# Kernel tuning notes

Hardware: AMD Instinct MI355X
Metric: run time of the kernel (lower is better)

Reference implementation:

```python
import math
import jax, jax.numpy as jnp
import numpy as np

B, T, D_MODEL = 4, 2048, 1024
H, HD = 16, 64            # head_dim = d_model // n_heads
NF = 128                  # n_features
EPS = 1e-6
INV_SQRT_NF = 1.0 / math.sqrt(NF)


def make_orf(key, head_dim, n_features, dtype=jnp.float32):
    """Orthogonal Random Features: QR-orthogonalized gaussian blocks, scaled by sqrt(d)."""
    n_blocks = math.ceil(n_features / head_dim)
    keys = jax.random.split(key, n_blocks)
    blocks = []
    for k in keys:
        g = jax.random.normal(k, (head_dim, head_dim), dtype)
        qm, _ = jnp.linalg.qr(g)
        blocks.append(qm)
    W = jnp.concatenate(blocks, axis=1)[:, :n_features]
    return W * jnp.asarray(math.sqrt(head_dim), dtype)


def setup_inputs() -> dict:
    key = jax.random.key(0)
    k0, k1, k2, k3, k4, k5 = jax.random.split(key, 6)
    s = 1.0 / math.sqrt(D_MODEL)  # torch Linear default init scale
    x = jax.random.normal(k0, (B, T, D_MODEL), jnp.float32)
    Wq = jax.random.uniform(k1, (D_MODEL, H * HD), jnp.float32, -s, s)
    Wk = jax.random.uniform(k2, (D_MODEL, H * HD), jnp.float32, -s, s)
    Wv = jax.random.uniform(k3, (D_MODEL, H * HD), jnp.float32, -s, s)
    Wo = jax.random.uniform(k4, (H * HD, D_MODEL), jnp.float32, -s, s)
    W_feat = make_orf(k5, HD, NF)  # (HD, NF), fresh random buffer (not learned)
    return {"x": x, "Wq": Wq, "Wk": Wk, "Wv": Wv, "Wo": Wo, "W_feat": W_feat}


def _favor_plus(x, W):
    """phi(x) = exp(x.W - ||x||^2/2) / sqrt(NF); x:(B,H,T,HD) -> (B,H,T,NF)."""
    sq = 0.5 * jnp.sum(x * x, axis=-1, keepdims=True)
    return jnp.exp(x @ W - sq) * INV_SQRT_NF


def _causal_linear_attention(qp, kp, v):
    """Causal linear attention scan. qp,kp:(B,H,T,NF), v:(B,H,T,HD) -> (B,H,T,HD)."""
    Bb, Hh = qp.shape[0], qp.shape[1]

    def step(carry, qkv):
        S, z = carry  # S:(B,H,NF,HD), z:(B,H,NF)
        q_t, k_t, v_t = qkv
        S = S + jnp.einsum('bhd,bhe->bhde', k_t, v_t)
        z = z + k_t
        num = jnp.einsum('bhd,bhde->bhe', q_t, S)
        den = jnp.einsum('bhd,bhd->bh', q_t, z) + EPS
        return (S, z), num / den[..., None]

    S0 = jnp.zeros((Bb, Hh, NF, HD), qp.dtype)
    z0 = jnp.zeros((Bb, Hh, NF), qp.dtype)
    xs = (jnp.moveaxis(qp, 2, 0), jnp.moveaxis(kp, 2, 0), jnp.moveaxis(v, 2, 0))
    _, ys = jax.lax.scan(step, (S0, z0), xs)  # ys: (T,B,H,HD)
    return jnp.moveaxis(ys, 0, 2)  # (B,H,T,HD)


def reference(x, Wq, Wk, Wv, Wo, W_feat):
    Bb, Tt, _ = x.shape

    def heads(W):
        return (x @ W).reshape(Bb, Tt, H, HD).transpose(0, 2, 1, 3)  # (B,H,T,HD)

    q, k, v = heads(Wq), heads(Wk), heads(Wv)
    qp = _favor_plus(q, W_feat)
    kp = _favor_plus(k, W_feat)
    y = _causal_linear_attention(qp, kp, v)           # (B,H,T,HD)
    y = y.transpose(0, 2, 1, 3).reshape(Bb, Tt, H * HD)
    return y @ Wo
```

## Files before the change

kernel.cpp:

```cpp
#include <hip/hip_runtime.h>
#include <hip/hip_bf16.h>

typedef unsigned int u32;
typedef unsigned short u16;
typedef __bf16 bf16x8 __attribute__((ext_vector_type(8)));
typedef float f32x4 __attribute__((ext_vector_type(4)));

__device__ __forceinline__ float b2f(u16 s){ union{u32 x; float f;} c; c.x = ((u32)s) << 16; return c.f; }
__device__ __forceinline__ float b2f_lo(u32 u){ union{u32 x; float f;} c; c.x = u << 16; return c.f; }
__device__ __forceinline__ float b2f_hi(u32 u){ union{u32 x; float f;} c; c.x = u & 0xFFFF0000u; return c.f; }
__device__ __forceinline__ u16 f2b(float f){
    union{float f; u32 u;} c; c.f = f;
    u32 r = c.u + 0x7FFFu + ((c.u >> 16) & 1u);
    return (u16)(r >> 16);
}
__device__ __forceinline__ u32 pk(float lo, float hi){
    return (u32)f2b(lo) | ((u32)f2b(hi) << 16);
}
__device__ __forceinline__ void gl_lds16(const u16* g, u16* l){
    __builtin_amdgcn_global_load_lds(
        (const __attribute__((address_space(1))) void*)g,
        (__attribute__((address_space(3))) void*)l, 16, 0, 0);
}
#define BARRIER() do { __builtin_amdgcn_s_barrier(); asm volatile("" ::: "memory"); } while(0)
#define SCB __builtin_amdgcn_sched_barrier(0)
#define LD8(p) (*reinterpret_cast<const bf16x8*>(p))


__global__ __launch_bounds__(256) void tobf16(const float* __restrict__ in, u16* __restrict__ out)
{
    size_t i = ((size_t)blockIdx.x * 256 + threadIdx.x) * 8;
    float4 a = *reinterpret_cast<const float4*>(in + i);
    float4 b = *reinterpret_cast<const float4*>(in + i + 4);
    uint4 v; v.x = pk(a.x, a.y); v.y = pk(a.z, a.w); v.z = pk(b.x, b.y); v.w = pk(b.z, b.w);
    *reinterpret_cast<uint4*>(out + i) = v;
}

__global__ __launch_bounds__(256) void transpose_all(const float* __restrict__ Wq, const float* __restrict__ Wk,
                                                     const float* __restrict__ Wv, const float* __restrict__ Wo,
                                                     u16* __restrict__ WTqkv, u16* __restrict__ WTo)
{
    const float* in; u16* out;
    switch (blockIdx.z){
        case 0:  in = Wq; out = WTqkv;           break;
        case 1:  in = Wk; out = WTqkv + 1048576; break;
        case 2:  in = Wv; out = WTqkv + 2097152; break;
        default: in = Wo; out = WTo;             break;
    }
    __shared__ u16 tile[64][72];
    int kb = blockIdx.x * 64, nb = blockIdx.y * 64, tid = threadIdx.x;
#pragma unroll
    for (int i = 0; i < 2; i++){
        int idx = tid + 256*i; int r = idx >> 3; int c8 = (idx & 7) * 8;
        const float* p = &in[(size_t)(kb + r)*1024 + nb + c8];
        float4 lo = *reinterpret_cast<const float4*>(p);
        float4 hi = *reinterpret_cast<const float4*>(p + 4);
        uint4 v;
        v.x = pk(lo.x, lo.y); v.y = pk(lo.z, lo.w);
        v.z = pk(hi.x, hi.y); v.w = pk(hi.z, hi.w);
        *reinterpret_cast<uint4*>(&tile[r][c8]) = v;
    }
    __syncthreads();
#pragma unroll
    for (int i = 0; i < 2; i++){
        int idx = tid + 256*i; int c = idx >> 3; int r8 = (idx & 7) * 8;
        u32 w[4];
#pragma unroll
        for (int j = 0; j < 4; j++)
            w[j] = (u32)tile[r8 + 2*j][c] | ((u32)tile[r8 + 2*j + 1][c] << 16);
        uint4 v; v.x = w[0]; v.y = w[1]; v.z = w[2]; v.w = w[3];
        *reinterpret_cast<uint4*>(&out[(size_t)(nb + c)*1024 + kb + r8]) = v;
    }
}

template<int MODE>
__global__ __launch_bounds__(512, 2) void gemm_1b(const u16* __restrict__ A, const u16* __restrict__ BT,
                                                  float* __restrict__ outf, u16* __restrict__ outh)
{
    __shared__ u16 lds[2][24576];
    const int tid = threadIdx.x;
    const int l = tid & 63, w = tid >> 6;
    const int wr = w >> 2, wc = w & 3;
    const int fr = l & 15, q = l >> 4;
    const int m0 = blockIdx.x * 128, n0 = blockIdx.y * 256;

    const int srow = tid >> 3;
    const int scol = ((tid & 7) ^ (srow & 7)) << 3;
    const u16* Ag = A  + (size_t)(m0 + srow) * 1024 + scol;
    const u16* Bg = BT + (size_t)(n0 + srow) * 1024 + scol;
    const int sd = tid * 8;

    const int colk0 = (q*8)      ^ ((fr & 7) << 3);
    const int colk1 = (32 + q*8) ^ ((fr & 7) << 3);
    const int aoff = (wr*64 + fr) * 64;
    const int boff = 8192 + (wc*64 + fr) * 64;

    f32x4 acc[4][4] = {};

    auto stgA = [&](int buf, int kt){
#pragma unroll
        for (int i = 0; i < 2; ++i)
            gl_lds16(Ag + (size_t)(i*64)*1024 + kt*64, &lds[buf][i*4096 + sd]);
    };
    auto stgB = [&](int buf, int kt){
#pragma unroll
        for (int j = 0; j < 4; ++j)
            gl_lds16(Bg + (size_t)(j*64)*1024 + kt*64, &lds[buf][8192 + j*4096 + sd]);
    };

    stgA(0, 0); stgB(0, 0); stgA(1, 1);
    asm volatile("s_waitcnt vmcnt(2)" ::: "memory");
    SCB;
    BARRIER();

#pragma unroll 1
    for (int uu = 0; uu < 8; ++uu){
#pragma unroll
        for (int par = 0; par < 2; ++par){
            const int u = 2*uu + par;
            u16* Lb = &lds[par][0];
            bf16x8 af[4][2], bf[4][2];

#pragma unroll
            for (int mt = 0; mt < 4; ++mt){
                af[mt][0] = LD8(Lb + aoff + mt*1024 + colk0);
                af[mt][1] = LD8(Lb + aoff + mt*1024 + colk1);
            }
#pragma unroll
            for (int nt = 0; nt < 4; ++nt){
                bf[nt][0] = LD8(Lb + boff + nt*1024 + colk0);
                bf[nt][1] = LD8(Lb + boff + nt*1024 + colk1);
            }
            if (u < 15) stgB(par ^ 1, u + 1);
            if (u < 14) stgA(par, u + 2);

            __builtin_amdgcn_s_setprio(1);
#pragma unroll
            for (int mt = 0; mt < 4; ++mt)
#pragma unroll
                for (int nt = 0; nt < 4; ++nt){
                    acc[mt][nt] = __builtin_amdgcn_mfma_f32_16x16x32_bf16(af[mt][0], bf[nt][0], acc[mt][nt], 0, 0, 0);
                    acc[mt][nt] = __builtin_amdgcn_mfma_f32_16x16x32_bf16(af[mt][1], bf[nt][1], acc[mt][nt], 0, 0, 0);
                }
            __builtin_amdgcn_s_setprio(0);
            SCB;
            if (u < 14){
                asm volatile("s_waitcnt vmcnt(2)" ::: "memory");
                SCB;
                BARRIER();
            } else if (u == 14){
                asm volatile("s_waitcnt vmcnt(0)" ::: "memory");
                SCB;
                BARRIER();
            }
        }
    }

#pragma unroll
    for (int mt = 0; mt < 4; ++mt){
        int row0 = m0 + wr*64 + mt*16 + q*4;
#pragma unroll
        for (int nt = 0; nt < 4; ++nt){
            int col = n0 + wc*64 + nt*16 + fr;
#pragma unroll
            for (int r = 0; r < 4; ++r){
                float val = acc[mt][nt][r];
                int row = row0 + r;
                if (MODE == 2){
                    outf[(size_t)row*1024 + col] = val;
                } else {
                    int which = col >> 10, colw = col & 1023;
                    int h = colw >> 6, d = colw & 63;
                    int bb = row >> 11, tt = row & 2047;
                    outh[(size_t)which*8388608 + (((size_t)(bb*16 + h))*2048 + tt)*64 + d] = f2b(val);
                }
            }
        }
    }
}

__global__ __launch_bounds__(256) void featmap_mfma(const u16* __restrict__ xh, const float* __restrict__ Wf,
                                                    u16* __restrict__ xp)
{
    __shared__ u16 Xl[128][72];
    __shared__ u16 Wft[128][72];
    __shared__ float sqp[128][8];
    __shared__ float sql[128];
    int tid = threadIdx.x;
    int lane = tid & 63, w = tid >> 6;
    int m = lane & 15, q = lane >> 4;
    const u16* xb = xh + (size_t)blockIdx.x * 128 * 64;
#pragma unroll
    for (int it = 0; it < 4; it++){
        int idx = tid + 256*it;
        int row = idx >> 3, c8 = (idx & 7) * 8;
        uint4 v = *reinterpret_cast<const uint4*>(xb + (size_t)row*64 + c8);
        *reinterpret_cast<uint4*>(&Xl[row][c8]) = v;
        u32 ww[4] = {v.x, v.y, v.z, v.w};
        float s = 0.f;
#pragma unroll
        for (int j = 0; j < 4; j++){
            float a = b2f_lo(ww[j]), bb = b2f_hi(ww[j]);
            s += a*a + bb*bb;
        }
        sqp[row][idx & 7] = s;
    }
#pragma unroll
    for (int it = 0; it < 8; it++){
        int idx = tid + 256*it;
        int d = idx >> 5, f4 = (idx & 31) * 4;
        float4 v = *reinterpret_cast<const float4*>(Wf + d*128 + f4);
        Wft[f4+0][d] = f2b(v.x); Wft[f4+1][d] = f2b(v.y);
        Wft[f4+2][d] = f2b(v.z); Wft[f4+3][d] = f2b(v.w);
    }
    __syncthreads();
    if (tid < 128){
        float s = 0.f;
#pragma unroll
        for (int j = 0; j < 8; j++) s += sqp[tid][j];
        sql[tid] = s;
    }
    f32x4 acc[2][8] = {};
#pragma unroll
    for (int ks = 0; ks < 2; ks++){
        bf16x8 af[2], bf[8];
#pragma unroll
        for (int mt = 0; mt < 2; mt++)
            af[mt] = *reinterpret_cast<const bf16x8*>(&Xl[32*w + mt*16 + m][ks*32 + q*8]);
#pragma unroll
        for (int nt = 0; nt < 8; nt++)
            bf[nt] = *reinterpret_cast<const bf16x8*>(&Wft[nt*16 + m][ks*32 + q*8]);
#pragma unroll
        for (int mt = 0; mt < 2; mt++)
#pragma unroll
            for (int nt = 0; nt < 8; nt++)
                acc[mt][nt] = __builtin_amdgcn_mfma_f32_16x16x32_bf16(af[mt], bf[nt], acc[mt][nt], 0, 0, 0);
    }
    __syncthreads();
    const float c = 0.08838834764831845f;
    u16* xpb = xp + (size_t)blockIdx.x * 128 * 128;
#pragma unroll
    for (int mt = 0; mt < 2; mt++){
#pragma unroll
        for (int r = 0; r < 4; r++){
            int t = 32*w + mt*16 + q*4 + r;
            float hs = 0.5f * sql[t];
#pragma unroll
            for (int nt = 0; nt < 8; nt++){
                int f = nt*16 + m;
                xpb[(size_t)t*128 + f] = f2b(__expf(fminf(acc[mt][nt][r] - hs, 60.f)) * c);
            }
        }
    }
}

struct FM1 { u16 Xl[128][72]; u16 Wft[128][72]; };
union  FMU { FM1 p1; u16 Kpt[128][136]; };
__global__ __launch_bounds__(256) void featmap_sum(const u16* __restrict__ kh, const float* __restrict__ Wf,
                                                   const u16* __restrict__ vh, u16* __restrict__ kp,
                                                   u16* __restrict__ Sa, float* __restrict__ zs)
{
    __shared__ FMU sm;
    __shared__ u16 Vt[64][136];
    __shared__ float sqp[128][8];
    __shared__ float sql[128];
    int blk = blockIdx.x, tid = threadIdx.x;
    int lane = tid & 63, w = tid >> 6;
    int m = lane & 15, q = lane >> 4;
    const u16* xb = kh + (size_t)blk * 128 * 64;
    const u16* vb = vh + (size_t)blk * 128 * 64;
#pragma unroll
    for (int it = 0; it < 4; it++){
        int idx = tid + 256*it;
        int row = idx >> 3, c8 = (idx & 7) * 8;
        uint4 v = *reinterpret_cast<const uint4*>(xb + (size_t)row*64 + c8);
        *reinterpret_cast<uint4*>(&sm.p1.Xl[row][c8]) = v;
        u32 ww[4] = {v.x, v.y, v.z, v.w};
        float s = 0.f;
#pragma unroll
        for (int j = 0; j < 4; j++){
            float a = b2f_lo(ww[j]), bb = b2f_hi(ww[j]);
            s += a*a + bb*bb;
        }
        sqp[row][idx & 7] = s;
    }
#pragma unroll
    for (int it = 0; it < 8; it++){
        int idx = tid + 256*it;
        int d = idx >> 5, f4 = (idx & 31) * 4;
        float4 v = *reinterpret_cast<const float4*>(Wf + d*128 + f4);
        sm.p1.Wft[f4+0][d] = f2b(v.x); sm.p1.Wft[f4+1][d] = f2b(v.y);
        sm.p1.Wft[f4+2][d] = f2b(v.z); sm.p1.Wft[f4+3][d] = f2b(v.w);
    }
#pragma unroll
    for (int it = 0; it < 4; it++){
        int idx = tid + 256*it;
        int t = idx >> 3, d8 = (idx & 7)*8;
        uint4 v = *reinterpret_cast<const uint4*>(vb + (size_t)t*64 + d8);
        u32 ww[4] = {v.x, v.y, v.z, v.w};
#pragma unroll
        for (int j = 0; j < 4; j++){
            Vt[d8 + 2*j][t]     = (u16)(ww[j] & 0xFFFFu);
            Vt[d8 + 2*j + 1][t] = (u16)(ww[j] >> 16);
        }
    }
    __syncthreads();
    if (tid < 128){
        float s = 0.f;
#pragma unroll
        for (int j = 0; j < 8; j++) s += sqp[tid][j];
        sql[tid] = s;
    }
    f32x4 acc[2][8] = {};
#pragma unroll
    for (int ks = 0; ks < 2; ks++){
        bf16x8 af[2], bf[8];
#pragma unroll
        for (int mt = 0; mt < 2; mt++)
            af[mt] = *reinterpret_cast<const bf16x8*>(&sm.p1.Xl[32*w + mt*16 + m][ks*32 + q*8]);
#pragma unroll
        for (int nt = 0; nt < 8; nt++)
            bf[nt] = *reinterpret_cast<const bf16x8*>(&sm.p1.Wft[nt*16 + m][ks*32 + q*8]);
#pragma unroll
        for (int mt = 0; mt < 2; mt++)
#pragma unroll
            for (int nt = 0; nt < 8; nt++)
                acc[mt][nt] = __builtin_amdgcn_mfma_f32_16x16x32_bf16(af[mt], bf[nt], acc[mt][nt], 0, 0, 0);
    }
    __syncthreads();
    const float c = 0.08838834764831845f;
    u16* xpb = kp + (size_t)blk * 128 * 128;
#pragma unroll
    for (int mt = 0; mt < 2; mt++){
#pragma unroll
        for (int r = 0; r < 4; r++){
            int t = 32*w + mt*16 + q*4 + r;
            float hs = 0.5f * sql[t];
#pragma unroll
            for (int nt = 0; nt < 8; nt++){
                int f = nt*16 + m;
                u16 pv = f2b(__expf(fminf(acc[mt][nt][r] - hs, 60.f)) * c);
                xpb[(size_t)t*128 + f] = pv;
                sm.Kpt[f][t] = pv;
            }
        }
    }
    __syncthreads();
    f32x4 acc2[8] = {};
#pragma unroll
    for (int ks = 0; ks < 4; ks++){
        bf16x8 af = *reinterpret_cast<const bf16x8*>(&Vt[16*w + m][ks*32 + q*8]);
        bf16x8 bf[8];
#pragma unroll
        for (int nt = 0; nt < 8; nt++)
            bf[nt] = *reinterpret_cast<const bf16x8*>(&sm.Kpt[nt*16 + m][ks*32 + q*8]);
#pragma unroll
        for (int nt = 0; nt < 8; nt++)
            acc2[nt] = __builtin_amdgcn_mfma_f32_16x16x32_bf16(af, bf[nt], acc2[nt], 0, 0, 0);
    }
    u16* Sb = Sa + (size_t)blk*8192;
#pragma unroll
    for (int nt = 0; nt < 8; nt++){
#pragma unroll
        for (int r = 0; r < 4; r++){
            int d = 16*w + q*4 + r;
            int f = nt*16 + m;
            Sb[(size_t)d*128 + f] = f2b(acc2[nt][r]);
        }
    }
    if (tid < 128){
        float z = 0.f;
#pragma unroll
        for (int t = 0; t < 128; t++) z += b2f(sm.Kpt[tid][t]);
        zs[(size_t)blk*128 + tid] = z;
    }
}

__global__ __launch_bounds__(256) void prefix_chunks(const u16* __restrict__ Sa, u16* __restrict__ Sb,
                                                     float* __restrict__ zs)
{
    int bh = blockIdx.x, seg = blockIdx.y, tid = threadIdx.x;
    const u16* src = Sa + (size_t)bh*16*8192;
    u16*       dst = Sb + (size_t)bh*16*8192;
#pragma unroll
    for (int it = 0; it < 4; it++){
        int e = seg*1024 + it*256 + tid;
        float run = 0.f;
#pragma unroll
        for (int c = 0; c < 16; c++){
            float v = b2f(src[(size_t)c*8192 + e]);
            dst[(size_t)c*8192 + e] = f2b(run);
            run += v;
        }
    }
    if (seg == 0 && tid < 128){
        float run = 0.f; float* zp = zs + (size_t)bh*16*128 + tid;
#pragma unroll
        for (int c = 0; c < 16; c++){ float v = zp[c*128]; zp[c*128] = run; run += v; }
    }
}

__global__ __launch_bounds__(512) void chunk_out(const u16* __restrict__ qp, const u16* __restrict__ kp,
                                                 const u16* __restrict__ vh, const u16* __restrict__ St,
                                                 const float* __restrict__ zs, u16* __restrict__ y2d)
{
    __shared__ u16 P[128][128];
    __shared__ u16 Vt[64][128];
    __shared__ u16 zl[128];
    int blk = blockIdx.x, tid = threadIdx.x;
    int lane = tid & 63, w = tid >> 6;
    int m = lane & 15, q = lane >> 4;
    int bh = blk >> 4, c = blk & 15;
    int b = bh >> 4, h = bh & 15, t0 = c*128;
    const u16* qpb = qp + ((size_t)bh*2048 + t0)*128;
    const u16* kpb = kp + ((size_t)bh*2048 + t0)*128;
    const u16* vb  = vh + ((size_t)bh*2048 + t0)*64;
    const u16* Stb = St + (size_t)blk*8192;
    const int xm = (m & 7) << 3;

    if (tid < 128) zl[tid] = f2b(zs[(size_t)blk*128 + tid]);
#pragma unroll
    for (int it = 0; it < 2; it++){
        int idx = tid + 512*it;
        int t = idx >> 3, d8 = (idx & 7)*8;
        uint4 v = *reinterpret_cast<const uint4*>(&vb[(size_t)t*64 + d8]);
        u32 ww[4] = {v.x, v.y, v.z, v.w};
#pragma unroll
        for (int j = 0; j < 4; j++){
            Vt[d8 + 2*j]    [t ^ ((2*j)     << 3)] = (u16)(ww[j] & 0xFFFFu);
            Vt[d8 + 2*j + 1][t ^ ((2*j + 1) << 3)] = (u16)(ww[j] >> 16);
        }
    }
    {
        int row = tid >> 2, c4 = tid & 3;
        int i = row >> 4, xr = (row & 7) << 3;
        for (int s2 = 16*(i + 1) + c4*2; s2 < 128; s2 += 8)
            *reinterpret_cast<u32*>(&P[row][s2 ^ xr]) = 0;
    }
    {
        static const unsigned char TIa[36] = {0,1,1,2,2,2,3,3,3,3,4,4,4,4,4,
                                              5,5,5,5,5,5,6,6,6,6,6,6,6,7,7,7,7,7,7,7,7};
        static const unsigned char TJa[36] = {0,0,1,0,1,2,0,1,2,3,0,1,2,3,4,
                                              0,1,2,3,4,5,0,1,2,3,4,5,6,0,1,2,3,4,5,6,7};
        for (int idx = w; idx < 36; idx += 8){
            int i = TIa[idx], j = TJa[idx];
            f32x4 a = {};
            const u16* arow = qpb + (size_t)(i*16 + m)*128 + q*8;
            const u16* brow = kpb + (size_t)(j*16 + m)*128 + q*8;
#pragma unroll
            for (int ks = 0; ks < 4; ks++){
                bf16x8 af = LD8(arow + ks*32);
                bf16x8 bf = LD8(brow + ks*32);
                a = __builtin_amdgcn_mfma_f32_16x16x32_bf16(af, bf, a, 0, 0, 0);
            }
            int scol = j*16 + m;
#pragma unroll
            for (int r = 0; r < 4; r++){
                int trow = i*16 + q*4 + r;
                P[trow][scol ^ ((trow & 7) << 3)] = (scol <= trow) ? f2b(a[r]) : (u16)0;
            }
        }
    }
    __syncthreads();
    f32x4 acc4[4] = {};
    f32x4 accd = {};
    bf16x8 ones;
#pragma unroll
    for (int i = 0; i < 8; i++) ones[i] = (__bf16)1.0f;
    for (int ks = 0; ks <= (w >> 1); ks++){
        bf16x8 af = LD8(&P[16*w + m][(ks*32 + q*8) ^ xm]);
        bf16x8 bf4[4];
#pragma unroll
        for (int nt = 0; nt < 4; nt++)
            bf4[nt] = LD8(&Vt[nt*16 + m][(ks*32 + q*8) ^ xm]);
#pragma unroll
        for (int nt = 0; nt < 4; nt++)
            acc4[nt] = __builtin_amdgcn_mfma_f32_16x16x32_bf16(af, bf4[nt], acc4[nt], 0, 0, 0);
        accd = __builtin_amdgcn_mfma_f32_16x16x32_bf16(af, ones, accd, 0, 0, 0);
    }
#pragma unroll
    for (int ks = 0; ks < 4; ks++){
        bf16x8 af = LD8(qpb + (size_t)(16*w + m)*128 + ks*32 + q*8);
        bf16x8 zf = LD8(&zl[ks*32 + q*8]);
        bf16x8 bf4[4];
#pragma unroll
        for (int nt = 0; nt < 4; nt++)
            bf4[nt] = LD8(Stb + (size_t)(nt*16 + m)*128 + ks*32 + q*8);
#pragma unroll
        for (int nt = 0; nt < 4; nt++)
            acc4[nt] = __builtin_amdgcn_mfma_f32_16x16x32_bf16(af, bf4[nt], acc4[nt], 0, 0, 0);
        accd = __builtin_amdgcn_mfma_f32_16x16x32_bf16(af, zf, accd, 0, 0, 0);
    }
#pragma unroll
    for (int nt = 0; nt < 4; nt++){
#pragma unroll
        for (int r = 0; r < 4; r++){
            int t = 16*w + q*4 + r;
            int d = nt*16 + m;
            float den = accd[r] + 1e-6f;
            y2d[((size_t)b*2048 + t0 + t)*1024 + h*64 + d] = f2b(acc4[nt][r] / den);
        }
    }
}

extern "C" void kernel_launch(void* const* d_in, const int* in_sizes, int n_in,
                              void* d_out, int out_size, void* d_ws, size_t ws_size,
                              hipStream_t stream)
{
    (void)in_sizes; (void)n_in; (void)out_size; (void)ws_size;
    const float* x  = (const float*)d_in[0];
    const float* Wq = (const float*)d_in[1];
    const float* Wk = (const float*)d_in[2];
    const float* Wv = (const float*)d_in[3];
    const float* Wo = (const float*)d_in[4];
    const float* Wf = (const float*)d_in[5];
    float* out = (float*)d_out;
    char* ws = (char*)d_ws;

    u16*   xh    = (u16*)  (ws + 0);
    u16*   Sa    = (u16*)  (ws + 0);
    u16*   qh    = (u16*)  (ws + 16777216);
    u16*   Sbp   = (u16*)  (ws + 16777216);
    u16*   kh    = (u16*)  (ws + 33554432);
    u16*   y2d   = (u16*)  (ws + 33554432);
    u16*   vh    = (u16*)  (ws + 50331648);
    u16*   qp    = (u16*)  (ws + 67108864);
    u16*   kp    = (u16*)  (ws + 100663296);
    u16*   WTqkv = (u16*)  (ws + 134217728);
    u16*   WTo   = (u16*)  (ws + 140509184);
    float* zs    = (float*)(ws + 142606336);

    tobf16<<<4096, 256, 0, stream>>>(x, xh);
    transpose_all<<<dim3(16, 16, 4), 256, 0, stream>>>(Wq, Wk, Wv, Wo, WTqkv, WTo);

    gemm_1b<3><<<dim3(64, 12), 512, 0, stream>>>(xh, WTqkv, nullptr, qh);

    featmap_mfma<<<1024, 256, 0, stream>>>(qh, Wf, qp);
    featmap_sum<<<1024, 256, 0, stream>>>(kh, Wf, vh, kp, Sa, zs);

    prefix_chunks<<<dim3(64, 8), 256, 0, stream>>>(Sa, Sbp, zs);
    chunk_out<<<1024, 512, 0, stream>>>(qp, kp, vh, Sbp, zs, y2d);

    gemm_1b<2><<<dim3(64, 4), 512, 0, stream>>>(y2d, WTo, out, nullptr);
}
```

Baseline: 283.9 us.

## Reorder chunk_out: inter-chunk state product first, double-buffer QK tile loads, new swizzle

```diff
diff --git a/kernel.cpp b/kernel.cpp
--- a/kernel.cpp
+++ b/kernel.cpp
@@ -25,6 +25,7 @@
 #define BARRIER() do { __builtin_amdgcn_s_barrier(); asm volatile("" ::: "memory"); } while(0)
 #define SCB __builtin_amdgcn_sched_barrier(0)
 #define LD8(p) (*reinterpret_cast<const bf16x8*>(p))
+#define SWZP(r) ((((r) ^ ((r) >> 3)) & 7) << 3)
 
 
 __global__ __launch_bounds__(256) void tobf16(const float* __restrict__ in, u16* __restrict__ out)
@@ -400,25 +401,23 @@
     }
 }
 
-__global__ __launch_bounds__(512) void chunk_out(const u16* __restrict__ qp, const u16* __restrict__ kp,
-                                                 const u16* __restrict__ vh, const u16* __restrict__ St,
-                                                 const float* __restrict__ zs, u16* __restrict__ y2d)
+__global__ __launch_bounds__(512, 4) void chunk_out(const u16* __restrict__ qp, const u16* __restrict__ kp,
+                                                    const u16* __restrict__ vh, const u16* __restrict__ St,
+                                                    const float* __restrict__ zs, u16* __restrict__ y2d)
 {
     __shared__ u16 P[128][128];
     __shared__ u16 Vt[64][128];
-    __shared__ u16 zl[128];
     int blk = blockIdx.x, tid = threadIdx.x;
     int lane = tid & 63, w = tid >> 6;
     int m = lane & 15, q = lane >> 4;
     int bh = blk >> 4, c = blk & 15;
     int b = bh >> 4, h = bh & 15, t0 = c*128;
-    const u16* qpb = qp + ((size_t)bh*2048 + t0)*128;
-    const u16* kpb = kp + ((size_t)bh*2048 + t0)*128;
-    const u16* vb  = vh + ((size_t)bh*2048 + t0)*64;
-    const u16* Stb = St + (size_t)blk*8192;
-    const int xm = (m & 7) << 3;
-
-    if (tid < 128) zl[tid] = f2b(zs[(size_t)blk*128 + tid]);
+    const u16*  qpb = qp + ((size_t)bh*2048 + t0)*128;
+    const u16*  kpb = kp + ((size_t)bh*2048 + t0)*128;
+    const u16*  vb  = vh + ((size_t)bh*2048 + t0)*64;
+    const u16*  Stb = St + (size_t)blk*8192;
+    const float* zsb = zs + (size_t)blk*128;
+
 #pragma unroll
     for (int it = 0; it < 2; it++){
         int idx = tid + 512*it;
@@ -427,69 +426,94 @@
         u32 ww[4] = {v.x, v.y, v.z, v.w};
 #pragma unroll
         for (int j = 0; j < 4; j++){
-            Vt[d8 + 2*j]    [t ^ ((2*j)     << 3)] = (u16)(ww[j] & 0xFFFFu);
-            Vt[d8 + 2*j + 1][t ^ ((2*j + 1) << 3)] = (u16)(ww[j] >> 16);
+            int d0 = d8 + 2*j, d1 = d0 + 1;
+            Vt[d0][t ^ SWZP(d0)] = (u16)(ww[j] & 0xFFFFu);
+            Vt[d1][t ^ SWZP(d1)] = (u16)(ww[j] >> 16);
         }
     }
     {
         int row = tid >> 2, c4 = tid & 3;
-        int i = row >> 4, xr = (row & 7) << 3;
+        int i = row >> 4, xr = SWZP(row);
         for (int s2 = 16*(i + 1) + c4*2; s2 < 128; s2 += 8)
             *reinterpret_cast<u32*>(&P[row][s2 ^ xr]) = 0;
     }
+
+    f32x4 acc4[4] = {};
+    f32x4 accd = {};
+#pragma unroll
+    for (int ks = 0; ks < 4; ks++){
+        bf16x8 af = LD8(qpb + (size_t)(16*w + m)*128 + ks*32 + q*8);
+        float4 z0 = *reinterpret_cast<const float4*>(zsb + ks*32 + q*8);
+        float4 z1 = *reinterpret_cast<const float4*>(zsb + ks*32 + q*8 + 4);
+        union { u32 u[4]; bf16x8 v; } zc;
+        zc.u[0] = pk(z0.x, z0.y); zc.u[1] = pk(z0.z, z0.w);
+        zc.u[2] = pk(z1.x, z1.y); zc.u[3] = pk(z1.z, z1.w);
+        bf16x8 bf4[4];
+#pragma unroll
+        for (int nt = 0; nt < 4; nt++)
+            bf4[nt] = LD8(Stb + (size_t)(nt*16 + m)*128 + ks*32 + q*8);
+#pragma unroll
+        for (int nt = 0; nt < 4; nt++)
+            acc4[nt] = __builtin_amdgcn_mfma_f32_16x16x32_bf16(af, bf4[nt], acc4[nt], 0, 0, 0);
+        accd = __builtin_amdgcn_mfma_f32_16x16x32_bf16(af, zc.v, accd, 0, 0, 0);
+    }
+
     {
         static const unsigned char TIa[36] = {0,1,1,2,2,2,3,3,3,3,4,4,4,4,4,
                                               5,5,5,5,5,5,6,6,6,6,6,6,6,7,7,7,7,7,7,7,7};
         static const unsigned char TJa[36] = {0,0,1,0,1,2,0,1,2,3,0,1,2,3,4,
                                               0,1,2,3,4,5,0,1,2,3,4,5,6,0,1,2,3,4,5,6,7};
-        for (int idx = w; idx < 36; idx += 8){
+        bf16x8 fa[2][4], fb[2][4];
+        auto ldtile = [&](int idx, bf16x8* A8, bf16x8* B8){
             int i = TIa[idx], j = TJa[idx];
+            const u16* ar = qpb + (size_t)(i*16 + m)*128 + q*8;
+            const u16* br = kpb + (size_t)(j*16 + m)*128 + q*8;
+#pragma unroll
+            for (int ks = 0; ks < 4; ks++){ A8[ks] = LD8(ar + ks*32); B8[ks] = LD8(br + ks*32); }
+        };
+        auto cptile = [&](int idx, bf16x8* A8, bf16x8* B8){
             f32x4 a = {};
-            const u16* arow = qpb + (size_t)(i*16 + m)*128 + q*8;
-            const u16* brow = kpb + (size_t)(j*16 + m)*128 + q*8;
-#pragma unroll
-            for (int ks = 0; ks < 4; ks++){
-                bf16x8 af = LD8(arow + ks*32);
-                bf16x8 bf = LD8(brow + ks*32);
-                a = __builtin_amdgcn_mfma_f32_16x16x32_bf16(af, bf, a, 0, 0, 0);
-            }
+#pragma unroll
+            for (int ks = 0; ks < 4; ks++)
+                a = __builtin_amdgcn_mfma_f32_16x16x32_bf16(A8[ks], B8[ks], a, 0, 0, 0);
+            int i = TIa[idx], j = TJa[idx];
             int scol = j*16 + m;
 #pragma unroll
             for (int r = 0; r < 4; r++){
                 int trow = i*16 + q*4 + r;
-                P[trow][scol ^ ((trow & 7) << 3)] = (scol <= trow) ? f2b(a[r]) : (u16)0;
-            }
-        }
-    }
-    __syncthreads();
-    f32x4 acc4[4] = {};
-    f32x4 accd = {};
+                P[trow][scol ^ SWZP(trow)] = (scol <= trow) ? f2b(a[r]) : (u16)0;
+            }
+        };
+        ldtile(w, fa[0], fb[0]);
+#pragma unroll
+        for (int itn = 0; itn < 4; ++itn){
+            if (itn < 3)      ldtile(w + (itn+1)*8, fa[(itn+1)&1], fb[(itn+1)&1]);
+            else if (w < 4)   ldtile(w + 32,        fa[(itn+1)&1], fb[(itn+1)&1]);
+            cptile(w + itn*8, fa[itn&1], fb[itn&1]);
+        }
+        if (w < 4) cptile(w + 32, fa[0], fb[0]);
+    }
+    __syncthreads();
+
     bf16x8 ones;
 #pragma unroll
     for (int i = 0; i < 8; i++) ones[i] = (__bf16)1.0f;
-    for (int ks = 0; ks <= (w >> 1); ks++){
-        bf16x8 af = LD8(&P[16*w + m][(ks*32 + q*8) ^ xm]);
-        bf16x8 bf4[4];
-#pragma unroll
-        for (int nt = 0; nt < 4; nt++)
-            bf4[nt] = LD8(&Vt[nt*16 + m][(ks*32 + q*8) ^ xm]);
-#pragma unroll
-        for (int nt = 0; nt < 4; nt++)
-            acc4[nt] = __builtin_amdgcn_mfma_f32_16x16x32_bf16(af, bf4[nt], acc4[nt], 0, 0, 0);
-        accd = __builtin_amdgcn_mfma_f32_16x16x32_bf16(af, ones, accd, 0, 0, 0);
-    }
-#pragma unroll
-    for (int ks = 0; ks < 4; ks++){
-        bf16x8 af = LD8(qpb + (size_t)(16*w + m)*128 + ks*32 + q*8);
-        bf16x8 zf = LD8(&zl[ks*32 + q*8]);
-        bf16x8 bf4[4];
-#pragma unroll
-        for (int nt = 0; nt < 4; nt++)
-            bf4[nt] = LD8(Stb + (size_t)(nt*16 + m)*128 + ks*32 + q*8);
-#pragma unroll
-        for (int nt = 0; nt < 4; nt++)
-            acc4[nt] = __builtin_amdgcn_mfma_f32_16x16x32_bf16(af, bf4[nt], acc4[nt], 0, 0, 0);
-        accd = __builtin_amdgcn_mfma_f32_16x16x32_bf16(af, zf, accd, 0, 0, 0);
+    {
+        int prow = 16*w + m, xp = SWZP(prow);
+        int xv[4];
+#pragma unroll
+        for (int nt = 0; nt < 4; nt++) xv[nt] = SWZP(nt*16 + m);
+        for (int ks = 0; ks <= (w >> 1); ks++){
+            bf16x8 af = LD8(&P[prow][(ks*32 + q*8) ^ xp]);
+            bf16x8 bf4[4];
+#pragma unroll
+            for (int nt = 0; nt < 4; nt++)
+                bf4[nt] = LD8(&Vt[nt*16 + m][(ks*32 + q*8) ^ xv[nt]]);
+#pragma unroll
+            for (int nt = 0; nt < 4; nt++)
+                acc4[nt] = __builtin_amdgcn_mfma_f32_16x16x32_bf16(af, bf4[nt], acc4[nt], 0, 0, 0);
+            accd = __builtin_amdgcn_mfma_f32_16x16x32_bf16(af, ones, accd, 0, 0, 0);
+        }
     }
 #pragma unroll
     for (int nt = 0; nt < 4; nt++){
```

Result: no change. 283.8 us (-0.1%).
